# Performance work log

Hardware: AMD Instinct MI355X
Metric: run time of the kernel (lower is better)

## Reference

```python
import jax, jax.numpy as jnp
import numpy as np

H = 1024  # hidden_dims

def _gru_scan(xs, h0, wih, whh, bih, bhh):
    # xs: (T, D_in); torch GRU gate order: r, z, n
    xp = xs @ wih.T + bih  # (T, 3H), precomputed input projection
    def step(h, xp_t):
        hh = h @ whh.T + bhh
        r = jax.nn.sigmoid(xp_t[:H] + hh[:H])
        z = jax.nn.sigmoid(xp_t[H:2 * H] + hh[H:2 * H])
        n = jnp.tanh(xp_t[2 * H:] + r * hh[2 * H:])
        h_new = (1.0 - z) * n + z * h
        return h_new, None
    h_last, _ = jax.lax.scan(step, h0, xp)
    return h_last

def _lstm_step(h_in, wih, bih, bhh):
    # single-step nn.LSTM(H, H) with zero initial (h0, c0): Whh terms vanish, biases remain.
    # torch LSTM gate order: i, f, g, o
    xp = h_in @ wih.T + bih + bhh  # (4H,)
    i = jax.nn.sigmoid(xp[:H])
    g = jnp.tanh(xp[2 * H:3 * H])
    o = jax.nn.sigmoid(xp[3 * H:])
    c = i * g  # f * c0 == 0
    return o * jnp.tanh(c)

def setup_inputs() -> dict:
    key = jax.random.key(0)
    ks = jax.random.split(key, 20)
    T, D_w, D_i = 8192, 32, 32
    s = 0.05
    inp = {
        "weather_window": jax.random.normal(ks[0], (T, 1, D_w), jnp.float32),
        "infect_window": jax.random.normal(ks[1], (T, 1, D_i), jnp.float32),
        "time_window": jax.random.uniform(ks[2], (T, 1), jnp.float32),
        "h_init": jax.random.normal(ks[3], (1, 1, H), jnp.float32),
        "enc_w1": jax.random.normal(ks[4], (512, 64), jnp.float32) * s,
        "enc_b1": jax.random.normal(ks[5], (512,), jnp.float32) * s,
        "enc_w2": jax.random.normal(ks[6], (1024, 512), jnp.float32) * s,
        "enc_b2": jax.random.normal(ks[7], (1024,), jnp.float32) * s,
        "gru_wih": jax.random.normal(ks[8], (3 * H, H), jnp.float32) * s,
        "gru_whh": jax.random.normal(ks[9], (3 * H, H), jnp.float32) * s,
        "gru_bih": jax.random.normal(ks[10], (3 * H,), jnp.float32) * s,
        "gru_bhh": jax.random.normal(ks[11], (3 * H,), jnp.float32) * s,
        "lstm_wih": jax.random.normal(ks[12], (4 * H, H), jnp.float32) * s,
        "lstm_bih": jax.random.normal(ks[13], (4 * H,), jnp.float32) * s,
        "lstm_bhh": jax.random.normal(ks[14], (4 * H,), jnp.float32) * s,
        "dec_w1": jax.random.normal(ks[15], (512, 1024), jnp.float32) * s,
        "dec_b1": jax.random.normal(ks[16], (512,), jnp.float32) * s,
        "dec_w2": jax.random.normal(ks[17], (8, 512), jnp.float32) * s,
        "dec_b2": jax.random.normal(ks[18], (8,), jnp.float32) * s,
    }
    return inp

def reference(weather_window, infect_window, time_window, h_init,
              enc_w1, enc_b1, enc_w2, enc_b2,
              gru_wih, gru_whh, gru_bih, gru_bhh,
              lstm_wih, lstm_bih, lstm_bhh,
              dec_w1, dec_b1, dec_w2, dec_b2):
    T = weather_window.shape[0]
    # use_diff_time = False branch
    data_window = jnp.concatenate([weather_window, infect_window], axis=2)  # (T,1,64)
    rev = data_window[::-1]  # flip(0)
    # Encoder FC stack
    x = jax.nn.relu(rev @ enc_w1.T + enc_b1)
    x = jax.nn.relu(x @ enc_w2.T + enc_b2)  # (T,1,H)
    # Encoder GRU -> final hidden state
    h_enc = _gru_scan(x[:, 0, :], h_init[0, 0], gru_wih, gru_whh, gru_bih, gru_bhh)  # (H,)
    def step(h, _):
        h_new = _lstm_step(h, lstm_wih, lstm_bih, lstm_bhh)
        return h_new, h_new
    _, hs_tail = jax.lax.scan(step, h_enc, None, length=T - 1)  # (T-1, H)
    hs = jnp.concatenate([h_enc[None, :], hs_tail], axis=0)  # (T, H)
    hs = hs[:, None, None, :]  # (T,1,1,H), matches torch.stack of (1,1,H)
    # Decoder FC stack
    y = jax.nn.relu(hs @ dec_w1.T + dec_b1)
    y = y @ dec_w2.T + dec_b2  # (T,1,1,8)
    return y
```

## Files before the change

kernel.cpp:

```cpp
#include <hip/hip_runtime.h>
#include <hip/hip_bf16.h>
#include <math.h>

#define T_STEPS 8192
#define HDIM    1024
#define GW      128
#define NSLOT   512
#define SLOT_PITCH 256
#define NREP    8
#define REP_STRIDE ((size_t)2 * NSLOT * SLOT_PITCH)

#define OFF_REV   ((size_t)0)
#define OFF_X1    ((size_t)2097152)
#define OFF_B     ((size_t)18874368)
#define OFF_C     ((size_t)52428800)
#define WS_NEEDED ((size_t)153092096)

typedef float f4 __attribute__((ext_vector_type(4)));

__device__ inline float sigm(float x)   { return 1.0f / (1.0f + __expf(-x)); }
__device__ inline float tanh_f(float x) { float e = __expf(2.0f * x); return 1.0f - 2.0f / (e + 1.0f); }

__device__ inline f4* slot_ptr(char* base, int rep, int b, int k) {
    return (f4*)(base + (size_t)rep * REP_STRIDE + ((size_t)b * NSLOT + k) * SLOT_PITCH);
}

__device__ inline void store_cohr(f4* p, f4 v) {
    asm volatile("global_store_dwordx4 %0, %1, off sc0 sc1"
                 :: "v"(p), "v"(v) : "memory");
}

__device__ inline void poll_pair(const f4* p, unsigned want, f4& a, f4& b) {
    for (;;) {
        f4 va, vb;
        asm volatile("global_load_dwordx4 %0, %2, off sc0 sc1\n\t"
                     "global_load_dwordx4 %1, %2, off offset:256 sc0 sc1\n\t"
                     "s_waitcnt vmcnt(0)"
                     : "=&v"(va), "=&v"(vb) : "v"(p) : "memory");
        if (__float_as_uint(va.w) == want && __float_as_uint(vb.w) == want) {
            a = va; b = vb; return;
        }
        __builtin_amdgcn_s_sleep(1);
    }
}

__global__ void build_rev(const float* __restrict__ wea, const float* __restrict__ inf,
                          float* __restrict__ rev) {
    int idx = blockIdx.x * blockDim.x + threadIdx.x;
    if (idx >= T_STEPS * 64) return;
    int t = idx >> 6, c = idx & 63;
    int ts = T_STEPS - 1 - t;
    rev[idx] = (c < 32) ? wea[ts * 32 + c] : inf[ts * 32 + (c - 32)];
}

__global__ void seed_slots(const float* __restrict__ h0, char* __restrict__ sb) {
    int i = blockIdx.x * blockDim.x + threadIdx.x;
    int rep = i >> 10;
    int j   = i & 1023;
    if (rep < NREP) {
        if (j < NSLOT) {
            f4 v;
            v.x = h0[2 * j]; v.y = h0[2 * j + 1]; v.z = 0.0f;
            v.w = __uint_as_float(0u);
            store_cohr(slot_ptr(sb, rep, 0, j), v);
        } else {
            f4 v;
            v.x = 0.f; v.y = 0.f; v.z = 0.f;
            v.w = __uint_as_float(0xFFFFFFFFu);
            store_cohr(slot_ptr(sb, rep, 1, j - NSLOT), v);
        }
    }
}

__global__ __launch_bounds__(256) void gemm_bias_act(
    const float* __restrict__ A, const float* __restrict__ W,
    const float* __restrict__ bias, float* __restrict__ C,
    int M, int N, int K, int relu)
{
    __shared__ float As[32][68];
    __shared__ float Ws[32][68];
    const int tid = threadIdx.x;
    const int tx = tid & 15, ty = tid >> 4;
    const int bm = blockIdx.y, bn = blockIdx.x;
    const float* Ab = A + (size_t)bm * 64 * K;
    const float* Wb = W + (size_t)bn * 64 * K;
    float acc[4][4] = {};

    for (int k0 = 0; k0 < K; k0 += 32) {
#pragma unroll
        for (int q = 0; q < 2; ++q) {
            int idx = tid * 2 + q;
            int row = idx >> 3;
            int kc  = (idx & 7) << 2;
            float4 av = *(const float4*)(Ab + (size_t)row * K + k0 + kc);
            As[kc + 0][row] = av.x; As[kc + 1][row] = av.y;
            As[kc + 2][row] = av.z; As[kc + 3][row] = av.w;
            float4 wv = *(const float4*)(Wb + (size_t)row * K + k0 + kc);
            Ws[kc + 0][row] = wv.x; Ws[kc + 1][row] = wv.y;
            Ws[kc + 2][row] = wv.z; Ws[kc + 3][row] = wv.w;
        }
        __syncthreads();
#pragma unroll
        for (int k = 0; k < 32; ++k) {
            float4 a = *(const float4*)&As[k][ty << 2];
            float4 b = *(const float4*)&Ws[k][tx << 2];
            acc[0][0] += a.x*b.x; acc[0][1] += a.x*b.y; acc[0][2] += a.x*b.z; acc[0][3] += a.x*b.w;
            acc[1][0] += a.y*b.x; acc[1][1] += a.y*b.y; acc[1][2] += a.y*b.z; acc[1][3] += a.y*b.w;
            acc[2][0] += a.z*b.x; acc[2][1] += a.z*b.y; acc[2][2] += a.z*b.z; acc[2][3] += a.z*b.w;
            acc[3][0] += a.w*b.x; acc[3][1] += a.w*b.y; acc[3][2] += a.w*b.z; acc[3][3] += a.w*b.w;
        }
        __syncthreads();
    }

    int m0 = bm * 64 + (ty << 2), n0 = bn * 64 + (tx << 2);
    float4 bv = *(const float4*)(bias + n0);
#pragma unroll
    for (int r = 0; r < 4; ++r) {
        float4 o;
        o.x = acc[r][0] + bv.x; o.y = acc[r][1] + bv.y;
        o.z = acc[r][2] + bv.z; o.w = acc[r][3] + bv.w;
        if (relu) {
            o.x = fmaxf(o.x, 0.f); o.y = fmaxf(o.y, 0.f);
            o.z = fmaxf(o.z, 0.f); o.w = fmaxf(o.w, 0.f);
        }
        *(float4*)(C + (size_t)(m0 + r) * N + n0) = o;
    }
}

__global__ __launch_bounds__(256, 1) void gru_scan(
    const float* __restrict__ whh,
    const float* __restrict__ bhh,
    const float* __restrict__ wih,
    const float* __restrict__ bih,
    const float* __restrict__ x2,
    char* __restrict__ sb)
{
    __shared__ float h_sh[2][HDIM];
    const int g = blockIdx.x, tid = threadIdx.x;
    const int w = tid >> 6, l = tid & 63;
    const int wv = g * 4 + w;
    const int rep = g & (NREP - 1);
    const int iA = 2 * wv, iB = iA + 1;
    const int rows[6] = { iA, HDIM + iA, 2*HDIM + iA, iB, HDIM + iB, 2*HDIM + iB };

    f4 Wf[6][4], Wi[6][4];
#pragma unroll
    for (int r = 0; r < 6; ++r) {
        const float* wr = whh + (size_t)rows[r] * HDIM + 4 * l;
        const float* wr2 = wih + (size_t)rows[r] * HDIM + 4 * l;
#pragma unroll
        for (int j = 0; j < 4; ++j) {
            Wf[r][j] = *(const f4*)(wr + 256 * j);
            Wi[r][j] = *(const f4*)(wr2 + 256 * j);
        }
    }
#pragma unroll
    for (int r = 0; r < 6; ++r)
#pragma unroll
        for (int j = 0; j < 4; ++j) {
            asm volatile("" : "+v"(Wf[r][j]));
            asm volatile("" : "+v"(Wi[r][j]));
        }

    float b0 = 0.f, b1 = 0.f, b2 = 0.f;
    float bi0 = 0.f, bi1 = 0.f, bi2 = 0.f;
    float xv0 = 0.f, xv1 = 0.f, xv2 = 0.f;
    int xrow = (l == 0) ? iA : iB;
    if (l < 2) {
        b0  = bhh[xrow]; b1  = bhh[HDIM + xrow]; b2  = bhh[2*HDIM + xrow];
        bi0 = bih[xrow]; bi1 = bih[HDIM + xrow]; bi2 = bih[2*HDIM + xrow];
    }

    {
        const float* xr = x2 + 4 * l;
        f4 x4p[4];
#pragma unroll
        for (int j = 0; j < 4; ++j) x4p[j] = *(const f4*)(xr + 256 * j);
        float xred[6];
#pragma unroll
        for (int r = 0; r < 6; ++r) {
            f4 p = Wi[r][0]*x4p[0] + Wi[r][1]*x4p[1] + Wi[r][2]*x4p[2] + Wi[r][3]*x4p[3];
            float v = p.x + p.y + p.z + p.w;
#pragma unroll
            for (int off = 32; off > 0; off >>= 1) v += __shfl_xor(v, off, 64);
            xred[r] = v;
        }
        if (l < 2) {
            xv0 = ((l == 0) ? xred[0] : xred[3]) + bi0;
            xv1 = ((l == 0) ? xred[1] : xred[4]) + bi1;
            xv2 = ((l == 0) ? xred[2] : xred[5]) + bi2;
        }
    }

    for (int t = 0; t < T_STEPS; ++t) {
        const int buf = t & 1;
        f4 sa, sb2;
        poll_pair(slot_ptr(sb, rep, buf, 2 * tid), (unsigned)t, sa, sb2);
        h_sh[buf][4*tid + 0] = sa.x;  h_sh[buf][4*tid + 1] = sa.y;
        h_sh[buf][4*tid + 2] = sb2.x; h_sh[buf][4*tid + 3] = sb2.y;
        __syncthreads();

        f4 h4[4];
#pragma unroll
        for (int j = 0; j < 4; ++j) h4[j] = *(const f4*)&h_sh[buf][256*j + 4*l];

        float red[6];
#pragma unroll
        for (int r = 0; r < 6; ++r) {
            f4 p = Wf[r][0]*h4[0] + Wf[r][1]*h4[1] + Wf[r][2]*h4[2] + Wf[r][3]*h4[3];
            float v = p.x + p.y + p.z + p.w;
#pragma unroll
            for (int off = 32; off > 0; off >>= 1) v += __shfl_xor(v, off, 64);
            red[r] = v;
        }

        float hn = 0.f;
        if (l < 2) {
            float rd0 = (l == 0) ? red[0] : red[3];
            float rd1 = (l == 0) ? red[1] : red[4];
            float rd2 = (l == 0) ? red[2] : red[5];
            float hh_r = rd0 + b0, hh_z = rd1 + b1, hh_n = rd2 + b2;
            float r_ = sigm(xv0 + hh_r);
            float z_ = sigm(xv1 + hh_z);
            float n_ = tanh_f(xv2 + r_ * hh_n);
            float hp = h_sh[buf][xrow];
            hn = (1.0f - z_) * n_ + z_ * hp;
        }
        float hAv = __shfl(hn, 0, 64);
        float hBv = __shfl(hn, 1, 64);
        if (l < NREP) {
            unsigned pub = (unsigned)(t + 1);
            f4 s; s.x = hAv; s.y = hBv; s.z = 0.0f; s.w = __uint_as_float(pub);
            store_cohr(slot_ptr(sb, l, (int)(pub & 1), wv), s);
        }
        if (t + 1 < T_STEPS) {
            const float* xr = x2 + (size_t)(t + 1) * HDIM + 4 * l;
            f4 x4p[4];
#pragma unroll
            for (int j = 0; j < 4; ++j) x4p[j] = *(const f4*)(xr + 256 * j);
            float xred[6];
#pragma unroll
            for (int r = 0; r < 6; ++r) {
                f4 p = Wi[r][0]*x4p[0] + Wi[r][1]*x4p[1] + Wi[r][2]*x4p[2] + Wi[r][3]*x4p[3];
                float v = p.x + p.y + p.z + p.w;
#pragma unroll
                for (int off = 32; off > 0; off >>= 1) v += __shfl_xor(v, off, 64);
                xred[r] = v;
            }
            if (l < 2) {
                xv0 = ((l == 0) ? xred[0] : xred[3]) + bi0;
                xv1 = ((l == 0) ? xred[1] : xred[4]) + bi1;
                xv2 = ((l == 0) ? xred[2] : xred[5]) + bi2;
            }
        }
    }
}

__global__ __launch_bounds__(256, 1) void lstm_scan(
    const float* __restrict__ wih,
    const float* __restrict__ bih,
    const float* __restrict__ bhh,
    const float* __restrict__ w1,
    const float* __restrict__ b1,
    char* __restrict__ sb,
    float* __restrict__ y1)
{
    __shared__ float h_sh[2][HDIM];
    const int g = blockIdx.x, tid = threadIdx.x;
    const int w = tid >> 6, l = tid & 63;
    const int wv = g * 4 + w;
    const int rep = g & (NREP - 1);
    const int iA = 2 * wv, iB = iA + 1;
    const int rows[6] = { iA, 2*HDIM + iA, 3*HDIM + iA, iB, 2*HDIM + iB, 3*HDIM + iB };

    f4 Wf[6][4];
#pragma unroll
    for (int r = 0; r < 6; ++r) {
        const float* wr = wih + (size_t)rows[r] * HDIM + 4 * l;
#pragma unroll
        for (int j = 0; j < 4; ++j) Wf[r][j] = *(const f4*)(wr + 256 * j);
    }
    f4 Wd[4];
    {
        const float* wr = w1 + (size_t)wv * HDIM + 4 * l;
#pragma unroll
        for (int j = 0; j < 4; ++j) Wd[j] = *(const f4*)(wr + 256 * j);
    }
#pragma unroll
    for (int r = 0; r < 6; ++r)
#pragma unroll
        for (int j = 0; j < 4; ++j)
            asm volatile("" : "+v"(Wf[r][j]));
#pragma unroll
    for (int j = 0; j < 4; ++j)
        asm volatile("" : "+v"(Wd[j]));

    const float db = b1[wv];

    float b0 = 0.f, b1_ = 0.f, b2 = 0.f;
    int xrow = (l == 0) ? iA : iB;
    if (l < 2) {
        b0  = bih[xrow]          + bhh[xrow];
        b1_ = bih[2*HDIM + xrow] + bhh[2*HDIM + xrow];
        b2  = bih[3*HDIM + xrow] + bhh[3*HDIM + xrow];
    }

    for (int s = 1; s <= T_STEPS; ++s) {
        const unsigned want = (unsigned)(8191 + s);
        const unsigned pub  = (unsigned)(8192 + s);
        const int buf = (int)(want & 1);
        f4 sa, sb2;
        poll_pair(slot_ptr(sb, rep, buf, 2 * tid), want, sa, sb2);
        h_sh[buf][4*tid + 0] = sa.x;  h_sh[buf][4*tid + 1] = sa.y;
        h_sh[buf][4*tid + 2] = sb2.x; h_sh[buf][4*tid + 3] = sb2.y;
        __syncthreads();

        f4 h4[4];
#pragma unroll
        for (int j = 0; j < 4; ++j) h4[j] = *(const f4*)&h_sh[buf][256*j + 4*l];

        if (s < T_STEPS) {
            float red[6];
#pragma unroll
            for (int r = 0; r < 6; ++r) {
                f4 p = Wf[r][0]*h4[0] + Wf[r][1]*h4[1] + Wf[r][2]*h4[2] + Wf[r][3]*h4[3];
                float v = p.x + p.y + p.z + p.w;
#pragma unroll
                for (int off = 32; off > 0; off >>= 1) v += __shfl_xor(v, off, 64);
                red[r] = v;
            }

            float hn = 0.f;
            if (l < 2) {
                float rd0 = (l == 0) ? red[0] : red[3];
                float rd1 = (l == 0) ? red[1] : red[4];
                float rd2 = (l == 0) ? red[2] : red[5];
                float i_ = sigm(rd0 + b0);
                float g_ = tanh_f(rd1 + b1_);
                float o_ = sigm(rd2 + b2);
                hn = o_ * tanh_f(i_ * g_);
            }
            float hAv = __shfl(hn, 0, 64);
            float hBv = __shfl(hn, 1, 64);
            if (l < NREP) {
                f4 sv; sv.x = hAv; sv.y = hBv; sv.z = 0.0f; sv.w = __uint_as_float(pub);
                store_cohr(slot_ptr(sb, l, (int)(pub & 1), wv), sv);
            }
        }

        {
            f4 p = Wd[0]*h4[0] + Wd[1]*h4[1] + Wd[2]*h4[2] + Wd[3]*h4[3];
            float v = p.x + p.y + p.z + p.w;
#pragma unroll
            for (int off = 32; off > 0; off >>= 1) v += __shfl_xor(v, off, 64);
            if (l == 0)
                y1[(size_t)(s - 1) * 512 + wv] = fmaxf(v + db, 0.f);
        }
    }
}

__global__ __launch_bounds__(256) void dec2_kernel(
    const float* __restrict__ y1,
    const float* __restrict__ w2,
    const float* __restrict__ b2,
    float* __restrict__ out)
{
    const int w = threadIdx.x >> 6, l = threadIdx.x & 63;
    const int t = blockIdx.x * 4 + w;
    const float* yr = y1 + (size_t)t * 512;
    float yv[8];
#pragma unroll
    for (int j = 0; j < 8; ++j) yv[j] = yr[l + 64 * j];
    float o[8];
#pragma unroll
    for (int n = 0; n < 8; ++n) {
        const float* wr = w2 + n * 512;
        float s = 0.f;
#pragma unroll
        for (int j = 0; j < 8; ++j) s += yv[j] * wr[l + 64 * j];
#pragma unroll
        for (int off = 32; off > 0; off >>= 1) s += __shfl_xor(s, off, 64);
        o[n] = s;
    }
    if (l == 0) {
#pragma unroll
        for (int n = 0; n < 8; ++n) out[(size_t)t * 8 + n] = o[n] + b2[n];
    }
}

extern "C" void kernel_launch(void* const* d_in, const int* in_sizes, int n_in,
                              void* d_out, int out_size, void* d_ws, size_t ws_size,
                              hipStream_t stream)
{
    const float* wea      = (const float*)d_in[0];
    const float* inf      = (const float*)d_in[1];
    const float* h_init   = (const float*)d_in[3];
    const float* enc_w1   = (const float*)d_in[4];
    const float* enc_b1   = (const float*)d_in[5];
    const float* enc_w2   = (const float*)d_in[6];
    const float* enc_b2   = (const float*)d_in[7];
    const float* gru_wih  = (const float*)d_in[8];
    const float* gru_whh  = (const float*)d_in[9];
    const float* gru_bih  = (const float*)d_in[10];
    const float* gru_bhh  = (const float*)d_in[11];
    const float* lstm_wih = (const float*)d_in[12];
    const float* lstm_bih = (const float*)d_in[13];
    const float* lstm_bhh = (const float*)d_in[14];
    const float* dec_w1   = (const float*)d_in[15];
    const float* dec_b1   = (const float*)d_in[16];
    const float* dec_w2   = (const float*)d_in[17];
    const float* dec_b2   = (const float*)d_in[18];

    if (ws_size < WS_NEEDED) return;

    char* ws = (char*)d_ws;
    float* rev   = (float*)(ws + OFF_REV);
    float* x1    = (float*)(ws + OFF_X1);
    float* x2    = (float*)(ws + OFF_B);
    float* y1    = (float*)(ws + OFF_C);
    char*  sb    = ws + OFF_X1;

    build_rev<<<(T_STEPS * 64) / 256, 256, 0, stream>>>(wea, inf, rev);

    gemm_bias_act<<<dim3(8, 128), 256, 0, stream>>>(rev, enc_w1, enc_b1, x1,
                                                    T_STEPS, 512, 64, 1);
    gemm_bias_act<<<dim3(16, 128), 256, 0, stream>>>(x1, enc_w2, enc_b2, x2,
                                                     T_STEPS, 1024, 512, 1);
    seed_slots<<<32, 256, 0, stream>>>(h_init, sb);
    gru_scan<<<GW, 256, 0, stream>>>(gru_whh, gru_bhh, gru_wih, gru_bih, x2, sb);
    lstm_scan<<<GW, 256, 0, stream>>>(lstm_wih, lstm_bih, lstm_bhh,
                                      dec_w1, dec_b1, sb, y1);

    dec2_kernel<<<T_STEPS / 4, 256, 0, stream>>>(y1, dec_w2, dec_b2, (float*)d_out);
}
```

Measured before the change: 38.00 ms.

## Overlap flag-poll latency with input projection and decoder work in scans

In the GRU scan, the first poll load for the hidden state is issued before the input-projection dot products for the current step, which now run while the load is in flight. The next step's x rows are prefetched during the recurrent matvec. In the LSTM scan, the decoder matvec for the previous step's hidden state now runs while the poll load is outstanding, and the last step is flushed after the loop. The aim is to hide cross-block synchronisation latency on the serial critical path, at the cost of extra registers held across the loop.

```diff
diff --git a/kernel.cpp b/kernel.cpp
--- a/kernel.cpp
+++ b/kernel.cpp
@@ -28,6 +28,15 @@
 __device__ inline void store_cohr(f4* p, f4 v) {
     asm volatile("global_store_dwordx4 %0, %1, off sc0 sc1"
                  :: "v"(p), "v"(v) : "memory");
+}
+
+__device__ inline void issue_pair(const f4* p, f4& a, f4& b) {
+    asm volatile("global_load_dwordx4 %0, %2, off sc0 sc1\n\t"
+                 "global_load_dwordx4 %1, %2, off offset:256 sc0 sc1"
+                 : "=&v"(a), "=&v"(b) : "v"(p) : "memory");
+}
+__device__ inline void wait_pair(f4& a, f4& b) {
+    asm volatile("s_waitcnt vmcnt(0)" : "+v"(a), "+v"(b) :: "memory");
 }
 
 __device__ inline void poll_pair(const f4* p, unsigned want, f4& a, f4& b) {
@@ -164,38 +173,50 @@
 
     float b0 = 0.f, b1 = 0.f, b2 = 0.f;
     float bi0 = 0.f, bi1 = 0.f, bi2 = 0.f;
-    float xv0 = 0.f, xv1 = 0.f, xv2 = 0.f;
     int xrow = (l == 0) ? iA : iB;
     if (l < 2) {
         b0  = bhh[xrow]; b1  = bhh[HDIM + xrow]; b2  = bhh[2*HDIM + xrow];
         bi0 = bih[xrow]; bi1 = bih[HDIM + xrow]; bi2 = bih[2*HDIM + xrow];
     }
 
+    f4 x4p[4];
     {
         const float* xr = x2 + 4 * l;
-        f4 x4p[4];
 #pragma unroll
         for (int j = 0; j < 4; ++j) x4p[j] = *(const f4*)(xr + 256 * j);
-        float xred[6];
-#pragma unroll
-        for (int r = 0; r < 6; ++r) {
-            f4 p = Wi[r][0]*x4p[0] + Wi[r][1]*x4p[1] + Wi[r][2]*x4p[2] + Wi[r][3]*x4p[3];
-            float v = p.x + p.y + p.z + p.w;
-#pragma unroll
-            for (int off = 32; off > 0; off >>= 1) v += __shfl_xor(v, off, 64);
-            xred[r] = v;
-        }
-        if (l < 2) {
-            xv0 = ((l == 0) ? xred[0] : xred[3]) + bi0;
-            xv1 = ((l == 0) ? xred[1] : xred[4]) + bi1;
-            xv2 = ((l == 0) ? xred[2] : xred[5]) + bi2;
-        }
+#pragma unroll
+        for (int j = 0; j < 4; ++j) asm volatile("" : "+v"(x4p[j]));
     }
 
     for (int t = 0; t < T_STEPS; ++t) {
         const int buf = t & 1;
+        const f4* pp = slot_ptr(sb, rep, buf, 2 * tid);
         f4 sa, sb2;
-        poll_pair(slot_ptr(sb, rep, buf, 2 * tid), (unsigned)t, sa, sb2);
+        issue_pair(pp, sa, sb2);
+
+        float xv0 = 0.f, xv1 = 0.f, xv2 = 0.f;
+        {
+            float xred[6];
+#pragma unroll
+            for (int r = 0; r < 6; ++r) {
+                f4 p = Wi[r][0]*x4p[0] + Wi[r][1]*x4p[1] + Wi[r][2]*x4p[2] + Wi[r][3]*x4p[3];
+                float v = p.x + p.y + p.z + p.w;
+#pragma unroll
+                for (int off = 32; off > 0; off >>= 1) v += __shfl_xor(v, off, 64);
+                xred[r] = v;
+            }
+            if (l < 2) {
+                xv0 = ((l == 0) ? xred[0] : xred[3]) + bi0;
+                xv1 = ((l == 0) ? xred[1] : xred[4]) + bi1;
+                xv2 = ((l == 0) ? xred[2] : xred[5]) + bi2;
+            }
+        }
+
+        wait_pair(sa, sb2);
+        if (!(__float_as_uint(sa.w) == (unsigned)t && __float_as_uint(sb2.w) == (unsigned)t)) {
+            __builtin_amdgcn_s_sleep(1);
+            poll_pair(pp, (unsigned)t, sa, sb2);
+        }
         h_sh[buf][4*tid + 0] = sa.x;  h_sh[buf][4*tid + 1] = sa.y;
         h_sh[buf][4*tid + 2] = sb2.x; h_sh[buf][4*tid + 3] = sb2.y;
         __syncthreads();
@@ -204,6 +225,13 @@
 #pragma unroll
         for (int j = 0; j < 4; ++j) h4[j] = *(const f4*)&h_sh[buf][256*j + 4*l];
 
+        {
+            int tn = (t + 1 < T_STEPS) ? (t + 1) : t;
+            const float* xr = x2 + (size_t)tn * HDIM + 4 * l;
+#pragma unroll
+            for (int j = 0; j < 4; ++j) x4p[j] = *(const f4*)(xr + 256 * j);
+        }
+
         float red[6];
 #pragma unroll
         for (int r = 0; r < 6; ++r) {
@@ -213,6 +241,9 @@
             for (int off = 32; off > 0; off >>= 1) v += __shfl_xor(v, off, 64);
             red[r] = v;
         }
+
+#pragma unroll
+        for (int j = 0; j < 4; ++j) asm volatile("" : "+v"(x4p[j]));
 
         float hn = 0.f;
         if (l < 2) {
@@ -232,26 +263,6 @@
             unsigned pub = (unsigned)(t + 1);
             f4 s; s.x = hAv; s.y = hBv; s.z = 0.0f; s.w = __uint_as_float(pub);
             store_cohr(slot_ptr(sb, l, (int)(pub & 1), wv), s);
-        }
-        if (t + 1 < T_STEPS) {
-            const float* xr = x2 + (size_t)(t + 1) * HDIM + 4 * l;
-            f4 x4p[4];
-#pragma unroll
-            for (int j = 0; j < 4; ++j) x4p[j] = *(const f4*)(xr + 256 * j);
-            float xred[6];
-#pragma unroll
-            for (int r = 0; r < 6; ++r) {
-                f4 p = Wi[r][0]*x4p[0] + Wi[r][1]*x4p[1] + Wi[r][2]*x4p[2] + Wi[r][3]*x4p[3];
-                float v = p.x + p.y + p.z + p.w;
-#pragma unroll
-                for (int off = 32; off > 0; off >>= 1) v += __shfl_xor(v, off, 64);
-                xred[r] = v;
-            }
-            if (l < 2) {
-                xv0 = ((l == 0) ? xred[0] : xred[3]) + bi0;
-                xv1 = ((l == 0) ? xred[1] : xred[4]) + bi1;
-                xv2 = ((l == 0) ? xred[2] : xred[5]) + bi2;
-            }
         }
     }
 }
@@ -305,12 +316,30 @@
         b2  = bih[3*HDIM + xrow] + bhh[3*HDIM + xrow];
     }
 
+    f4 hp4[4];
+
     for (int s = 1; s <= T_STEPS; ++s) {
         const unsigned want = (unsigned)(8191 + s);
         const unsigned pub  = (unsigned)(8192 + s);
         const int buf = (int)(want & 1);
+        const f4* pp = slot_ptr(sb, rep, buf, 2 * tid);
         f4 sa, sb2;
-        poll_pair(slot_ptr(sb, rep, buf, 2 * tid), want, sa, sb2);
+        issue_pair(pp, sa, sb2);
+
+        if (s > 1) {
+            f4 p = Wd[0]*hp4[0] + Wd[1]*hp4[1] + Wd[2]*hp4[2] + Wd[3]*hp4[3];
+            float v = p.x + p.y + p.z + p.w;
+#pragma unroll
+            for (int off = 32; off > 0; off >>= 1) v += __shfl_xor(v, off, 64);
+            if (l == 0)
+                y1[(size_t)(s - 2) * 512 + wv] = fmaxf(v + db, 0.f);
+        }
+
+        wait_pair(sa, sb2);
+        if (!(__float_as_uint(sa.w) == want && __float_as_uint(sb2.w) == want)) {
+            __builtin_amdgcn_s_sleep(1);
+            poll_pair(pp, want, sa, sb2);
+        }
         h_sh[buf][4*tid + 0] = sa.x;  h_sh[buf][4*tid + 1] = sa.y;
         h_sh[buf][4*tid + 2] = sb2.x; h_sh[buf][4*tid + 3] = sb2.y;
         __syncthreads();
@@ -347,15 +376,17 @@
                 store_cohr(slot_ptr(sb, l, (int)(pub & 1), wv), sv);
             }
         }
-
-        {
-            f4 p = Wd[0]*h4[0] + Wd[1]*h4[1] + Wd[2]*h4[2] + Wd[3]*h4[3];
-            float v = p.x + p.y + p.z + p.w;
-#pragma unroll
-            for (int off = 32; off > 0; off >>= 1) v += __shfl_xor(v, off, 64);
-            if (l == 0)
-                y1[(size_t)(s - 1) * 512 + wv] = fmaxf(v + db, 0.f);
-        }
+#pragma unroll
+        for (int j = 0; j < 4; ++j) hp4[j] = h4[j];
+    }
+
+    {
+        f4 p = Wd[0]*hp4[0] + Wd[1]*hp4[1] + Wd[2]*hp4[2] + Wd[3]*hp4[3];
+        float v = p.x + p.y + p.z + p.w;
+#pragma unroll
+        for (int off = 32; off > 0; off >>= 1) v += __shfl_xor(v, off, 64);
+        if (l == 0)
+            y1[(size_t)(T_STEPS - 1) * 512 + wv] = fmaxf(v + db, 0.f);
     }
 }
 
```

Result: slower. 44.42 ms (+16.9%).
